# Optimization experiments

Hardware: AMD Instinct MI355X
Metric: run time of the kernel (lower is better)

The kernel has to match this reference:

```python
import jax, jax.numpy as jnp
import numpy as np


def setup_inputs() -> dict:
    key = jax.random.key(0)
    ks = jax.random.split(key, 5)
    B, N, H, S, D = 1, 256, 4, 256, 32
    q = jax.random.normal(ks[0], (B, N, H, S, D), dtype=jnp.float32)
    k = jax.random.normal(ks[1], (B, N, H, S, D), dtype=jnp.float32)
    v = jax.random.normal(ks[2], (B, N, H, S, D), dtype=jnp.float32)
    mask_bias = jax.random.normal(ks[3], (B, N, 1, 1, S), dtype=jnp.float32)
    triangle_bias = jax.random.normal(ks[4], (B, 1, H, S, S), dtype=jnp.float32)
    return {"q": q, "k": k, "v": v, "mask_bias": mask_bias, "triangle_bias": triangle_bias}


def reference(q, k, v, mask_bias, triangle_bias):
    # q,k,v: [B, N, H, S, D]; mask_bias: [B, N, 1, 1, S]; triangle_bias: [B, 1, H, S, S]
    D = q.shape[-1]
    sm_scale = 1.0 / jnp.sqrt(jnp.asarray(D, dtype=q.dtype))
    # scores: [B, N, H, S, S] (query index s attends over key index t)
    scores = jnp.einsum("bnhsd,bnhtd->bnhst", q, k) * sm_scale
    scores = scores + mask_bias + triangle_bias  # broadcast add of both biases
    p = jax.nn.softmax(scores, axis=-1)
    out = jnp.einsum("bnhst,bnhtd->bnhsd", p, v)
    return out
```

## Files before the change

kernel.cpp:

```cpp
#include <hip/hip_runtime.h>

typedef __bf16 bf16;
typedef bf16 bf16x2 __attribute__((ext_vector_type(2)));
typedef bf16 bf16x4 __attribute__((ext_vector_type(4)));
typedef bf16 bf16x8 __attribute__((ext_vector_type(8)));
typedef float f32x4 __attribute__((ext_vector_type(4)));
typedef float f32x16 __attribute__((ext_vector_type(16)));
typedef int i32x2 __attribute__((ext_vector_type(2)));
typedef int i32x4 __attribute__((ext_vector_type(4)));

#define SEQ 256
#define DH  32
#define VT_PAD 264
#define KB_PAD 40

static __device__ __forceinline__ int pk2(float a, float b) {
    bf16x2 t; t[0] = (bf16)a; t[1] = (bf16)b;
    return __builtin_bit_cast(int, t);
}

template<int G>
static __device__ __forceinline__ i32x2 pgrp(f32x16 cf, f32x4 tg, f32x4 mk, float& lp) {
    constexpr float K1    = 0.17677669529663687f * 1.44269504088896f;
    constexpr float LOG2E = 1.44269504088896f;
    float p0 = __builtin_amdgcn_exp2f(fmaf(cf[4*G+0], K1, fmaf(tg[0], LOG2E, mk[0])));
    float p1 = __builtin_amdgcn_exp2f(fmaf(cf[4*G+1], K1, fmaf(tg[1], LOG2E, mk[1])));
    float p2 = __builtin_amdgcn_exp2f(fmaf(cf[4*G+2], K1, fmaf(tg[2], LOG2E, mk[2])));
    float p3 = __builtin_amdgcn_exp2f(fmaf(cf[4*G+3], K1, fmaf(tg[3], LOG2E, mk[3])));
    lp += (p0 + p1) + (p2 + p3);
    i32x2 r; r[0] = pk2(p0, p1); r[1] = pk2(p2, p3);
    return r;
}

static __device__ __forceinline__ void frags(i32x2 a0, i32x2 a1, i32x2 a2, i32x2 a3,
                                             bf16x8& f0, bf16x8& f1) {
    i32x2 s0 = __builtin_amdgcn_permlane32_swap(a0[0], a1[0], false, false);
    i32x2 s1 = __builtin_amdgcn_permlane32_swap(a0[1], a1[1], false, false);
    i32x2 s2 = __builtin_amdgcn_permlane32_swap(a2[0], a3[0], false, false);
    i32x2 s3 = __builtin_amdgcn_permlane32_swap(a2[1], a3[1], false, false);
    i32x4 w0 = {s0[0], s1[0], s0[1], s1[1]};
    i32x4 w1 = {s2[0], s3[0], s2[1], s3[1]};
    f0 = __builtin_bit_cast(bf16x8, w0);
    f1 = __builtin_bit_cast(bf16x8, w1);
}

__global__ __launch_bounds__(256, 2) void attn_mfma_kernel(
    const float* __restrict__ q,
    const float* __restrict__ k,
    const float* __restrict__ v,
    const float* __restrict__ mask_bias,
    const float* __restrict__ tri_bias,
    float* __restrict__ out)
{
    __shared__ bf16 Vt[DH][VT_PAD];
    __shared__ bf16 Kb[SEQ][KB_PAD];
    __shared__ float Ml[SEQ];

    const int tid  = threadIdx.x;
    const int wave = tid >> 6;
    const int lane = tid & 63;
    const int l31  = lane & 31;
    const int hi   = lane >> 5;

    const int inst = blockIdx.x;
    const int n    = inst >> 2;
    const int h    = inst & 3;

    const float* qb = q + (size_t)inst * SEQ * DH;
    const float* kb = k + (size_t)inst * SEQ * DH;
    const float* vb = v + (size_t)inst * SEQ * DH;
    const float* mb = mask_bias + (size_t)n * SEQ;
    const float* tb = tri_bias + (size_t)h * SEQ * SEQ;

    constexpr float LOG2E = 1.44269504088896f;

    const int sbase = wave * 64;

    const float* trow0 = tb + (size_t)(sbase + l31) * SEQ + 4 * hi;
    const float* trow1 = trow0 + 32 * SEQ;

    f32x4 tp0 = *(const f32x4*)(trow0 + 0);
    f32x4 tp1 = *(const f32x4*)(trow0 + 8);
    f32x4 tp2 = *(const f32x4*)(trow0 + 16);
    f32x4 tp3 = *(const f32x4*)(trow0 + 24);

    bf16x8 qf00, qf01, qf10, qf11;
    {
        const float* p0 = qb + (size_t)(sbase + l31) * DH + hi * 8;
        const float* p1 = qb + (size_t)(sbase + 32 + l31) * DH + hi * 8;
        f32x4 a, b;
        bf16x8 f;
        a = ((const f32x4*)p0)[0]; b = ((const f32x4*)p0)[1];
        f[0]=(bf16)a[0]; f[1]=(bf16)a[1]; f[2]=(bf16)a[2]; f[3]=(bf16)a[3];
        f[4]=(bf16)b[0]; f[5]=(bf16)b[1]; f[6]=(bf16)b[2]; f[7]=(bf16)b[3];
        qf00 = f;
        a = ((const f32x4*)(p0 + 16))[0]; b = ((const f32x4*)(p0 + 16))[1];
        f[0]=(bf16)a[0]; f[1]=(bf16)a[1]; f[2]=(bf16)a[2]; f[3]=(bf16)a[3];
        f[4]=(bf16)b[0]; f[5]=(bf16)b[1]; f[6]=(bf16)b[2]; f[7]=(bf16)b[3];
        qf01 = f;
        a = ((const f32x4*)p1)[0]; b = ((const f32x4*)p1)[1];
        f[0]=(bf16)a[0]; f[1]=(bf16)a[1]; f[2]=(bf16)a[2]; f[3]=(bf16)a[3];
        f[4]=(bf16)b[0]; f[5]=(bf16)b[1]; f[6]=(bf16)b[2]; f[7]=(bf16)b[3];
        qf10 = f;
        a = ((const f32x4*)(p1 + 16))[0]; b = ((const f32x4*)(p1 + 16))[1];
        f[0]=(bf16)a[0]; f[1]=(bf16)a[1]; f[2]=(bf16)a[2]; f[3]=(bf16)a[3];
        f[4]=(bf16)b[0]; f[5]=(bf16)b[1]; f[6]=(bf16)b[2]; f[7]=(bf16)b[3];
        qf11 = f;
    }

    #pragma unroll
    for (int i = 0; i < 8; ++i) {
        int idx = i * 256 + tid;
        int t   = idx >> 3;
        int d4  = (idx & 7) * 4;
        f32x4 tv = ((const f32x4*)vb)[idx];
        Vt[d4 + 0][t] = (bf16)tv[0];
        Vt[d4 + 1][t] = (bf16)tv[1];
        Vt[d4 + 2][t] = (bf16)tv[2];
        Vt[d4 + 3][t] = (bf16)tv[3];
        f32x4 tk = ((const f32x4*)kb)[idx];
        bf16x4 kk;
        kk[0]=(bf16)tk[0]; kk[1]=(bf16)tk[1]; kk[2]=(bf16)tk[2]; kk[3]=(bf16)tk[3];
        *(bf16x4*)&Kb[t][d4] = kk;
    }
    Ml[tid] = mb[tid] * LOG2E;
    __syncthreads();

    f32x16 oacc0 = {}, oacc1 = {};
    float lp0 = 0.f, lp1 = 0.f;
    const f32x16 z16 = {};

    for (int c = 0; c < 8; ++c) {
        const int tb0 = c * 32;

        f32x4 u0 = *(const f32x4*)(trow1 + tb0 + 0);
        f32x4 u1 = *(const f32x4*)(trow1 + tb0 + 8);
        f32x4 u2 = *(const f32x4*)(trow1 + tb0 + 16);
        f32x4 u3 = *(const f32x4*)(trow1 + tb0 + 24);

        bf16x8 kf0 = *(const bf16x8*)&Kb[tb0 + l31][hi * 8];
        bf16x8 kf1 = *(const bf16x8*)&Kb[tb0 + l31][16 + hi * 8];

        f32x4 mk0 = *(const f32x4*)&Ml[tb0 +  0 + 4 * hi];
        f32x4 mk1 = *(const f32x4*)&Ml[tb0 +  8 + 4 * hi];
        f32x4 mk2 = *(const f32x4*)&Ml[tb0 + 16 + 4 * hi];
        f32x4 mk3 = *(const f32x4*)&Ml[tb0 + 24 + 4 * hi];

        f32x16 cf = __builtin_amdgcn_mfma_f32_32x32x16_bf16(kf0, qf00, z16, 0, 0, 0);
        cf = __builtin_amdgcn_mfma_f32_32x32x16_bf16(kf1, qf01, cf, 0, 0, 0);

        i32x2 a0 = pgrp<0>(cf, tp0, mk0, lp0);
        i32x2 a1 = pgrp<1>(cf, tp1, mk1, lp0);
        i32x2 a2 = pgrp<2>(cf, tp2, mk2, lp0);
        i32x2 a3 = pgrp<3>(cf, tp3, mk3, lp0);

        if (c < 7) {
            tp0 = *(const f32x4*)(trow0 + tb0 + 32);
            tp1 = *(const f32x4*)(trow0 + tb0 + 40);
            tp2 = *(const f32x4*)(trow0 + tb0 + 48);
            tp3 = *(const f32x4*)(trow0 + tb0 + 56);
        }

        bf16x8 pa0, pa1;
        frags(a0, a1, a2, a3, pa0, pa1);

        bf16x8 vf0 = *(const bf16x8*)&Vt[l31][tb0 + hi * 8];
        bf16x8 vf1 = *(const bf16x8*)&Vt[l31][tb0 + 16 + hi * 8];

        oacc0 = __builtin_amdgcn_mfma_f32_32x32x16_bf16(pa0, vf0, oacc0, 0, 0, 0);
        oacc0 = __builtin_amdgcn_mfma_f32_32x32x16_bf16(pa1, vf1, oacc0, 0, 0, 0);

        cf = __builtin_amdgcn_mfma_f32_32x32x16_bf16(kf0, qf10, z16, 0, 0, 0);
        cf = __builtin_amdgcn_mfma_f32_32x32x16_bf16(kf1, qf11, cf, 0, 0, 0);

        a0 = pgrp<0>(cf, u0, mk0, lp1);
        a1 = pgrp<1>(cf, u1, mk1, lp1);
        a2 = pgrp<2>(cf, u2, mk2, lp1);
        a3 = pgrp<3>(cf, u3, mk3, lp1);

        bf16x8 pb0, pb1;
        frags(a0, a1, a2, a3, pb0, pb1);

        oacc1 = __builtin_amdgcn_mfma_f32_32x32x16_bf16(pb0, vf0, oacc1, 0, 0, 0);
        oacc1 = __builtin_amdgcn_mfma_f32_32x32x16_bf16(pb1, vf1, oacc1, 0, 0, 0);
    }

    lp0 += __shfl_xor(lp0, 32);
    lp1 += __shfl_xor(lp1, 32);
    const float li0 = 1.0f / lp0;
    const float li1 = 1.0f / lp1;

    float* ob = out + (size_t)inst * SEQ * DH;
    #pragma unroll
    for (int r = 0; r < 16; ++r) {
        const int srow = (r & 3) + 8 * (r >> 2) + 4 * hi;
        float i0 = __shfl(li0, srow);
        float i1 = __shfl(li1, srow);
        ob[(size_t)(sbase + srow) * DH + l31]      = oacc0[r] * i0;
        ob[(size_t)(sbase + 32 + srow) * DH + l31] = oacc1[r] * i1;
    }
}

extern "C" void kernel_launch(void* const* d_in, const int* in_sizes, int n_in,
                              void* d_out, int out_size, void* d_ws, size_t ws_size,
                              hipStream_t stream) {
    const float* q    = (const float*)d_in[0];
    const float* k    = (const float*)d_in[1];
    const float* v    = (const float*)d_in[2];
    const float* mask = (const float*)d_in[3];
    const float* tri  = (const float*)d_in[4];
    float* out = (float*)d_out;

    attn_mfma_kernel<<<dim3(256 * 4), dim3(256), 0, stream>>>(q, k, v, mask, tri, out);
}
```

Before: 158.5 us.

## Split each attention instance across two blocks and stream K from global

```diff
diff --git a/kernel.cpp b/kernel.cpp
--- a/kernel.cpp
+++ b/kernel.cpp
@@ -12,11 +12,17 @@
 #define SEQ 256
 #define DH  32
 #define VT_PAD 264
-#define KB_PAD 40
 
 static __device__ __forceinline__ int pk2(float a, float b) {
     bf16x2 t; t[0] = (bf16)a; t[1] = (bf16)b;
     return __builtin_bit_cast(int, t);
+}
+
+static __device__ __forceinline__ bf16x8 cvt8(f32x4 a, f32x4 b) {
+    bf16x8 f;
+    f[0]=(bf16)a[0]; f[1]=(bf16)a[1]; f[2]=(bf16)a[2]; f[3]=(bf16)a[3];
+    f[4]=(bf16)b[0]; f[5]=(bf16)b[1]; f[6]=(bf16)b[2]; f[7]=(bf16)b[3];
+    return f;
 }
 
 template<int G>
@@ -44,7 +50,7 @@
     f1 = __builtin_bit_cast(bf16x8, w1);
 }
 
-__global__ __launch_bounds__(256, 2) void attn_mfma_kernel(
+__global__ __launch_bounds__(256, 4) void attn_mfma_kernel(
     const float* __restrict__ q,
     const float* __restrict__ k,
     const float* __restrict__ v,
@@ -53,7 +59,6 @@
     float* __restrict__ out)
 {
     __shared__ bf16 Vt[DH][VT_PAD];
-    __shared__ bf16 Kb[SEQ][KB_PAD];
     __shared__ float Ml[SEQ];
 
     const int tid  = threadIdx.x;
@@ -62,7 +67,10 @@
     const int l31  = lane & 31;
     const int hi   = lane >> 5;
 
-    const int inst = blockIdx.x;
+    const int bid  = blockIdx.x;
+    const int swz  = (bid & 7) * 256 + (bid >> 3);
+    const int inst = swz >> 1;
+    const int halfb= swz & 1;
     const int n    = inst >> 2;
     const int h    = inst & 3;
 
@@ -74,38 +82,25 @@
 
     constexpr float LOG2E = 1.44269504088896f;
 
-    const int sbase = wave * 64;
+    const int qbase = halfb * 128 + wave * 32;
 
-    const float* trow0 = tb + (size_t)(sbase + l31) * SEQ + 4 * hi;
-    const float* trow1 = trow0 + 32 * SEQ;
+    const float* trow = tb + (size_t)(qbase + l31) * SEQ + 4 * hi;
 
-    f32x4 tp0 = *(const f32x4*)(trow0 + 0);
-    f32x4 tp1 = *(const f32x4*)(trow0 + 8);
-    f32x4 tp2 = *(const f32x4*)(trow0 + 16);
-    f32x4 tp3 = *(const f32x4*)(trow0 + 24);
+    const float* kp0 = kb + (size_t)l31 * DH + hi * 8;
+    f32x4 kA = ((const f32x4*)kp0)[0];
+    f32x4 kB = ((const f32x4*)kp0)[1];
+    f32x4 kC = ((const f32x4*)(kp0 + 16))[0];
+    f32x4 kD = ((const f32x4*)(kp0 + 16))[1];
+    f32x4 tp0 = *(const f32x4*)(trow + 0);
+    f32x4 tp1 = *(const f32x4*)(trow + 8);
+    f32x4 tp2 = *(const f32x4*)(trow + 16);
+    f32x4 tp3 = *(const f32x4*)(trow + 24);
 
-    bf16x8 qf00, qf01, qf10, qf11;
+    bf16x8 qf0, qf1;
     {
-        const float* p0 = qb + (size_t)(sbase + l31) * DH + hi * 8;
-        const float* p1 = qb + (size_t)(sbase + 32 + l31) * DH + hi * 8;
-        f32x4 a, b;
-        bf16x8 f;
-        a = ((const f32x4*)p0)[0]; b = ((const f32x4*)p0)[1];
-        f[0]=(bf16)a[0]; f[1]=(bf16)a[1]; f[2]=(bf16)a[2]; f[3]=(bf16)a[3];
-        f[4]=(bf16)b[0]; f[5]=(bf16)b[1]; f[6]=(bf16)b[2]; f[7]=(bf16)b[3];
-        qf00 = f;
-        a = ((const f32x4*)(p0 + 16))[0]; b = ((const f32x4*)(p0 + 16))[1];
-        f[0]=(bf16)a[0]; f[1]=(bf16)a[1]; f[2]=(bf16)a[2]; f[3]=(bf16)a[3];
-        f[4]=(bf16)b[0]; f[5]=(bf16)b[1]; f[6]=(bf16)b[2]; f[7]=(bf16)b[3];
-        qf01 = f;
-        a = ((const f32x4*)p1)[0]; b = ((const f32x4*)p1)[1];
-        f[0]=(bf16)a[0]; f[1]=(bf16)a[1]; f[2]=(bf16)a[2]; f[3]=(bf16)a[3];
-        f[4]=(bf16)b[0]; f[5]=(bf16)b[1]; f[6]=(bf16)b[2]; f[7]=(bf16)b[3];
-        qf10 = f;
-        a = ((const f32x4*)(p1 + 16))[0]; b = ((const f32x4*)(p1 + 16))[1];
-        f[0]=(bf16)a[0]; f[1]=(bf16)a[1]; f[2]=(bf16)a[2]; f[3]=(bf16)a[3];
-        f[4]=(bf16)b[0]; f[5]=(bf16)b[1]; f[6]=(bf16)b[2]; f[7]=(bf16)b[3];
-        qf11 = f;
+        const float* p = qb + (size_t)(qbase + l31) * DH + hi * 8;
+        qf0 = cvt8(((const f32x4*)p)[0], ((const f32x4*)p)[1]);
+        qf1 = cvt8(((const f32x4*)(p + 16))[0], ((const f32x4*)(p + 16))[1]);
     }
 
     #pragma unroll
@@ -118,86 +113,64 @@
         Vt[d4 + 1][t] = (bf16)tv[1];
         Vt[d4 + 2][t] = (bf16)tv[2];
         Vt[d4 + 3][t] = (bf16)tv[3];
-        f32x4 tk = ((const f32x4*)kb)[idx];
-        bf16x4 kk;
-        kk[0]=(bf16)tk[0]; kk[1]=(bf16)tk[1]; kk[2]=(bf16)tk[2]; kk[3]=(bf16)tk[3];
-        *(bf16x4*)&Kb[t][d4] = kk;
     }
     Ml[tid] = mb[tid] * LOG2E;
     __syncthreads();
 
-    f32x16 oacc0 = {}, oacc1 = {};
-    float lp0 = 0.f, lp1 = 0.f;
+    f32x16 oacc = {};
+    float lp = 0.f;
     const f32x16 z16 = {};
 
     for (int c = 0; c < 8; ++c) {
         const int tb0 = c * 32;
 
-        f32x4 u0 = *(const f32x4*)(trow1 + tb0 + 0);
-        f32x4 u1 = *(const f32x4*)(trow1 + tb0 + 8);
-        f32x4 u2 = *(const f32x4*)(trow1 + tb0 + 16);
-        f32x4 u3 = *(const f32x4*)(trow1 + tb0 + 24);
+        bf16x8 kf0 = cvt8(kA, kB);
+        bf16x8 kf1 = cvt8(kC, kD);
+        f32x4 t0 = tp0, t1 = tp1, t2 = tp2, t3 = tp3;
 
-        bf16x8 kf0 = *(const bf16x8*)&Kb[tb0 + l31][hi * 8];
-        bf16x8 kf1 = *(const bf16x8*)&Kb[tb0 + l31][16 + hi * 8];
+        if (c < 7) {
+            const float* kp = kb + (size_t)(tb0 + 32 + l31) * DH + hi * 8;
+            kA = ((const f32x4*)kp)[0];
+            kB = ((const f32x4*)kp)[1];
+            kC = ((const f32x4*)(kp + 16))[0];
+            kD = ((const f32x4*)(kp + 16))[1];
+            tp0 = *(const f32x4*)(trow + tb0 + 32);
+            tp1 = *(const f32x4*)(trow + tb0 + 40);
+            tp2 = *(const f32x4*)(trow + tb0 + 48);
+            tp3 = *(const f32x4*)(trow + tb0 + 56);
+        }
 
         f32x4 mk0 = *(const f32x4*)&Ml[tb0 +  0 + 4 * hi];
         f32x4 mk1 = *(const f32x4*)&Ml[tb0 +  8 + 4 * hi];
         f32x4 mk2 = *(const f32x4*)&Ml[tb0 + 16 + 4 * hi];
         f32x4 mk3 = *(const f32x4*)&Ml[tb0 + 24 + 4 * hi];
 
-        f32x16 cf = __builtin_amdgcn_mfma_f32_32x32x16_bf16(kf0, qf00, z16, 0, 0, 0);
-        cf = __builtin_amdgcn_mfma_f32_32x32x16_bf16(kf1, qf01, cf, 0, 0, 0);
+        f32x16 cf = __builtin_amdgcn_mfma_f32_32x32x16_bf16(kf0, qf0, z16, 0, 0, 0);
+        cf = __builtin_amdgcn_mfma_f32_32x32x16_bf16(kf1, qf1, cf, 0, 0, 0);
 
-        i32x2 a0 = pgrp<0>(cf, tp0, mk0, lp0);
-        i32x2 a1 = pgrp<1>(cf, tp1, mk1, lp0);
-        i32x2 a2 = pgrp<2>(cf, tp2, mk2, lp0);
-        i32x2 a3 = pgrp<3>(cf, tp3, mk3, lp0);
-
-        if (c < 7) {
-            tp0 = *(const f32x4*)(trow0 + tb0 + 32);
-            tp1 = *(const f32x4*)(trow0 + tb0 + 40);
-            tp2 = *(const f32x4*)(trow0 + tb0 + 48);
-            tp3 = *(const f32x4*)(trow0 + tb0 + 56);
-        }
-
+        i32x2 a0 = pgrp<0>(cf, t0, mk0, lp);
+        i32x2 a1 = pgrp<1>(cf, t1, mk1, lp);
+        i32x2 a2 = pgrp<2>(cf, t2, mk2, lp);
+        i32x2 a3 = pgrp<3>(cf, t3, mk3, lp);
         bf16x8 pa0, pa1;
         frags(a0, a1, a2, a3, pa0, pa1);
 
         bf16x8 vf0 = *(const bf16x8*)&Vt[l31][tb0 + hi * 8];
         bf16x8 vf1 = *(const bf16x8*)&Vt[l31][tb0 + 16 + hi * 8];
 
-        oacc0 = __builtin_amdgcn_mfma_f32_32x32x16_bf16(pa0, vf0, oacc0, 0, 0, 0);
-        oacc0 = __builtin_amdgcn_mfma_f32_32x32x16_bf16(pa1, vf1, oacc0, 0, 0, 0);
-
-        cf = __builtin_amdgcn_mfma_f32_32x32x16_bf16(kf0, qf10, z16, 0, 0, 0);
-        cf = __builtin_amdgcn_mfma_f32_32x32x16_bf16(kf1, qf11, cf, 0, 0, 0);
-
-        a0 = pgrp<0>(cf, u0, mk0, lp1);
-        a1 = pgrp<1>(cf, u1, mk1, lp1);
-        a2 = pgrp<2>(cf, u2, mk2, lp1);
-        a3 = pgrp<3>(cf, u3, mk3, lp1);
-
-        bf16x8 pb0, pb1;
-        frags(a0, a1, a2, a3, pb0, pb1);
-
-        oacc1 = __builtin_amdgcn_mfma_f32_32x32x16_bf16(pb0, vf0, oacc1, 0, 0, 0);
-        oacc1 = __builtin_amdgcn_mfma_f32_32x32x16_bf16(pb1, vf1, oacc1, 0, 0, 0);
+        oacc = __builtin_amdgcn_mfma_f32_32x32x16_bf16(pa0, vf0, oacc, 0, 0, 0);
+        oacc = __builtin_amdgcn_mfma_f32_32x32x16_bf16(pa1, vf1, oacc, 0, 0, 0);
     }
 
-    lp0 += __shfl_xor(lp0, 32);
-    lp1 += __shfl_xor(lp1, 32);
-    const float li0 = 1.0f / lp0;
-    const float li1 = 1.0f / lp1;
+    lp += __shfl_xor(lp, 32);
+    const float linv = 1.0f / lp;
 
     float* ob = out + (size_t)inst * SEQ * DH;
     #pragma unroll
     for (int r = 0; r < 16; ++r) {
         const int srow = (r & 3) + 8 * (r >> 2) + 4 * hi;
-        float i0 = __shfl(li0, srow);
-        float i1 = __shfl(li1, srow);
-        ob[(size_t)(sbase + srow) * DH + l31]      = oacc0[r] * i0;
-        ob[(size_t)(sbase + 32 + srow) * DH + l31] = oacc1[r] * i1;
+        float invr = __shfl(linv, srow);
+        ob[(size_t)(qbase + srow) * DH + l31] = oacc[r] * invr;
     }
 }
 
@@ -211,5 +184,5 @@
     const float* tri  = (const float*)d_in[4];
     float* out = (float*)d_out;
 
-    attn_mfma_kernel<<<dim3(256 * 4), dim3(256), 0, stream>>>(q, k, v, mask, tri, out);
+    attn_mfma_kernel<<<dim3(2048), dim3(256), 0, stream>>>(q, k, v, mask, tri, out);
 }
```

Result: slower. 266.1 us (+67.9%).

## Stream K fragments from global into registers and raise MFMA wave priority

Applied to the files above, without the earlier changes.

```diff
diff --git a/kernel.cpp b/kernel.cpp
--- a/kernel.cpp
+++ b/kernel.cpp
@@ -12,11 +12,17 @@
 #define SEQ 256
 #define DH  32
 #define VT_PAD 264
-#define KB_PAD 40
 
 static __device__ __forceinline__ int pk2(float a, float b) {
     bf16x2 t; t[0] = (bf16)a; t[1] = (bf16)b;
     return __builtin_bit_cast(int, t);
+}
+
+static __device__ __forceinline__ bf16x8 cvt8(f32x4 a, f32x4 b) {
+    bf16x8 f;
+    f[0]=(bf16)a[0]; f[1]=(bf16)a[1]; f[2]=(bf16)a[2]; f[3]=(bf16)a[3];
+    f[4]=(bf16)b[0]; f[5]=(bf16)b[1]; f[6]=(bf16)b[2]; f[7]=(bf16)b[3];
+    return f;
 }
 
 template<int G>
@@ -53,7 +59,6 @@
     float* __restrict__ out)
 {
     __shared__ bf16 Vt[DH][VT_PAD];
-    __shared__ bf16 Kb[SEQ][KB_PAD];
     __shared__ float Ml[SEQ];
 
     const int tid  = threadIdx.x;
@@ -79,6 +84,11 @@
     const float* trow0 = tb + (size_t)(sbase + l31) * SEQ + 4 * hi;
     const float* trow1 = trow0 + 32 * SEQ;
 
+    const float* kp0 = kb + (size_t)l31 * DH + hi * 8;
+    f32x4 kA = ((const f32x4*)kp0)[0];
+    f32x4 kB = ((const f32x4*)kp0)[1];
+    f32x4 kC = ((const f32x4*)(kp0 + 16))[0];
+    f32x4 kD = ((const f32x4*)(kp0 + 16))[1];
     f32x4 tp0 = *(const f32x4*)(trow0 + 0);
     f32x4 tp1 = *(const f32x4*)(trow0 + 8);
     f32x4 tp2 = *(const f32x4*)(trow0 + 16);
@@ -88,24 +98,10 @@
     {
         const float* p0 = qb + (size_t)(sbase + l31) * DH + hi * 8;
         const float* p1 = qb + (size_t)(sbase + 32 + l31) * DH + hi * 8;
-        f32x4 a, b;
-        bf16x8 f;
-        a = ((const f32x4*)p0)[0]; b = ((const f32x4*)p0)[1];
-        f[0]=(bf16)a[0]; f[1]=(bf16)a[1]; f[2]=(bf16)a[2]; f[3]=(bf16)a[3];
-        f[4]=(bf16)b[0]; f[5]=(bf16)b[1]; f[6]=(bf16)b[2]; f[7]=(bf16)b[3];
-        qf00 = f;
-        a = ((const f32x4*)(p0 + 16))[0]; b = ((const f32x4*)(p0 + 16))[1];
-        f[0]=(bf16)a[0]; f[1]=(bf16)a[1]; f[2]=(bf16)a[2]; f[3]=(bf16)a[3];
-        f[4]=(bf16)b[0]; f[5]=(bf16)b[1]; f[6]=(bf16)b[2]; f[7]=(bf16)b[3];
-        qf01 = f;
-        a = ((const f32x4*)p1)[0]; b = ((const f32x4*)p1)[1];
-        f[0]=(bf16)a[0]; f[1]=(bf16)a[1]; f[2]=(bf16)a[2]; f[3]=(bf16)a[3];
-        f[4]=(bf16)b[0]; f[5]=(bf16)b[1]; f[6]=(bf16)b[2]; f[7]=(bf16)b[3];
-        qf10 = f;
-        a = ((const f32x4*)(p1 + 16))[0]; b = ((const f32x4*)(p1 + 16))[1];
-        f[0]=(bf16)a[0]; f[1]=(bf16)a[1]; f[2]=(bf16)a[2]; f[3]=(bf16)a[3];
-        f[4]=(bf16)b[0]; f[5]=(bf16)b[1]; f[6]=(bf16)b[2]; f[7]=(bf16)b[3];
-        qf11 = f;
+        qf00 = cvt8(((const f32x4*)p0)[0], ((const f32x4*)p0)[1]);
+        qf01 = cvt8(((const f32x4*)(p0 + 16))[0], ((const f32x4*)(p0 + 16))[1]);
+        qf10 = cvt8(((const f32x4*)p1)[0], ((const f32x4*)p1)[1]);
+        qf11 = cvt8(((const f32x4*)(p1 + 16))[0], ((const f32x4*)(p1 + 16))[1]);
     }
 
     #pragma unroll
@@ -118,10 +114,6 @@
         Vt[d4 + 1][t] = (bf16)tv[1];
         Vt[d4 + 2][t] = (bf16)tv[2];
         Vt[d4 + 3][t] = (bf16)tv[3];
-        f32x4 tk = ((const f32x4*)kb)[idx];
-        bf16x4 kk;
-        kk[0]=(bf16)tk[0]; kk[1]=(bf16)tk[1]; kk[2]=(bf16)tk[2]; kk[3]=(bf16)tk[3];
-        *(bf16x4*)&Kb[t][d4] = kk;
     }
     Ml[tid] = mb[tid] * LOG2E;
     __syncthreads();
@@ -132,57 +124,67 @@
 
     for (int c = 0; c < 8; ++c) {
         const int tb0 = c * 32;
+
+        bf16x8 kf0 = cvt8(kA, kB);
+        bf16x8 kf1 = cvt8(kC, kD);
+        f32x4 t0 = tp0, t1 = tp1, t2 = tp2, t3 = tp3;
 
         f32x4 u0 = *(const f32x4*)(trow1 + tb0 + 0);
         f32x4 u1 = *(const f32x4*)(trow1 + tb0 + 8);
         f32x4 u2 = *(const f32x4*)(trow1 + tb0 + 16);
         f32x4 u3 = *(const f32x4*)(trow1 + tb0 + 24);
 
-        bf16x8 kf0 = *(const bf16x8*)&Kb[tb0 + l31][hi * 8];
-        bf16x8 kf1 = *(const bf16x8*)&Kb[tb0 + l31][16 + hi * 8];
-
-        f32x4 mk0 = *(const f32x4*)&Ml[tb0 +  0 + 4 * hi];
-        f32x4 mk1 = *(const f32x4*)&Ml[tb0 +  8 + 4 * hi];
-        f32x4 mk2 = *(const f32x4*)&Ml[tb0 + 16 + 4 * hi];
-        f32x4 mk3 = *(const f32x4*)&Ml[tb0 + 24 + 4 * hi];
-
-        f32x16 cf = __builtin_amdgcn_mfma_f32_32x32x16_bf16(kf0, qf00, z16, 0, 0, 0);
-        cf = __builtin_amdgcn_mfma_f32_32x32x16_bf16(kf1, qf01, cf, 0, 0, 0);
-
-        i32x2 a0 = pgrp<0>(cf, tp0, mk0, lp0);
-        i32x2 a1 = pgrp<1>(cf, tp1, mk1, lp0);
-        i32x2 a2 = pgrp<2>(cf, tp2, mk2, lp0);
-        i32x2 a3 = pgrp<3>(cf, tp3, mk3, lp0);
-
         if (c < 7) {
+            const float* kp = kb + (size_t)(tb0 + 32 + l31) * DH + hi * 8;
+            kA = ((const f32x4*)kp)[0];
+            kB = ((const f32x4*)kp)[1];
+            kC = ((const f32x4*)(kp + 16))[0];
+            kD = ((const f32x4*)(kp + 16))[1];
             tp0 = *(const f32x4*)(trow0 + tb0 + 32);
             tp1 = *(const f32x4*)(trow0 + tb0 + 40);
             tp2 = *(const f32x4*)(trow0 + tb0 + 48);
             tp3 = *(const f32x4*)(trow0 + tb0 + 56);
         }
 
+        bf16x8 vf0 = *(const bf16x8*)&Vt[l31][tb0 + hi * 8];
+        bf16x8 vf1 = *(const bf16x8*)&Vt[l31][tb0 + 16 + hi * 8];
+
+        f32x4 mk0 = *(const f32x4*)&Ml[tb0 +  0 + 4 * hi];
+        f32x4 mk1 = *(const f32x4*)&Ml[tb0 +  8 + 4 * hi];
+        f32x4 mk2 = *(const f32x4*)&Ml[tb0 + 16 + 4 * hi];
+        f32x4 mk3 = *(const f32x4*)&Ml[tb0 + 24 + 4 * hi];
+
+        __builtin_amdgcn_s_setprio(1);
+        f32x16 cf = __builtin_amdgcn_mfma_f32_32x32x16_bf16(kf0, qf00, z16, 0, 0, 0);
+        cf = __builtin_amdgcn_mfma_f32_32x32x16_bf16(kf1, qf01, cf, 0, 0, 0);
+        __builtin_amdgcn_s_setprio(0);
+
+        i32x2 a0 = pgrp<0>(cf, t0, mk0, lp0);
+        i32x2 a1 = pgrp<1>(cf, t1, mk1, lp0);
+        i32x2 a2 = pgrp<2>(cf, t2, mk2, lp0);
+        i32x2 a3 = pgrp<3>(cf, t3, mk3, lp0);
         bf16x8 pa0, pa1;
         frags(a0, a1, a2, a3, pa0, pa1);
 
-        bf16x8 vf0 = *(const bf16x8*)&Vt[l31][tb0 + hi * 8];
-        bf16x8 vf1 = *(const bf16x8*)&Vt[l31][tb0 + 16 + hi * 8];
-
+        __builtin_amdgcn_s_setprio(1);
         oacc0 = __builtin_amdgcn_mfma_f32_32x32x16_bf16(pa0, vf0, oacc0, 0, 0, 0);
         oacc0 = __builtin_amdgcn_mfma_f32_32x32x16_bf16(pa1, vf1, oacc0, 0, 0, 0);
 
         cf = __builtin_amdgcn_mfma_f32_32x32x16_bf16(kf0, qf10, z16, 0, 0, 0);
         cf = __builtin_amdgcn_mfma_f32_32x32x16_bf16(kf1, qf11, cf, 0, 0, 0);
+        __builtin_amdgcn_s_setprio(0);
 
         a0 = pgrp<0>(cf, u0, mk0, lp1);
         a1 = pgrp<1>(cf, u1, mk1, lp1);
         a2 = pgrp<2>(cf, u2, mk2, lp1);
         a3 = pgrp<3>(cf, u3, mk3, lp1);
-
         bf16x8 pb0, pb1;
         frags(a0, a1, a2, a3, pb0, pb1);
 
+        __builtin_amdgcn_s_setprio(1);
         oacc1 = __builtin_amdgcn_mfma_f32_32x32x16_bf16(pb0, vf0, oacc1, 0, 0, 0);
         oacc1 = __builtin_amdgcn_mfma_f32_32x32x16_bf16(pb1, vf1, oacc1, 0, 0, 0);
+        __builtin_amdgcn_s_setprio(0);
     }
 
     lp0 += __shfl_xor(lp0, 32);
```

Result: slower. 168.1 us (+6.1%).
